# Optimization experiments

Hardware: AMD Instinct MI355X
Metric: run time of the kernel (lower is better)

## Reference

```python
import jax, jax.numpy as jnp
import numpy as np

MAX_ITER = 3  # module default init kwarg
B, S = 16, 128


def setup_inputs() -> dict:
    key = jax.random.key(0)
    k1, k2, k3 = jax.random.split(key, 3)
    s_span = jax.random.normal(k1, (B, S, S), dtype=jnp.float32)
    s_pair = jax.random.normal(k2, (B, S, S, S), dtype=jnp.float32)
    mask = jax.random.randint(k3, (B, S, S), 0, 2).astype(jnp.bool_)
    return {"s_span": s_span, "s_pair": s_pair, "mask": mask}


def reference(s_span, s_pair, mask):
    # Faithful batch-first translation of MFVIConstituency.mfvi + sigmoid.
    # torch code works in [S, S, B] layout; here we keep [B, S, S].
    seq_len = mask.shape[1]
    idx = jnp.arange(seq_len)
    # ls[i,j]=min(i,j), rs[i,j]=max(i,j) (stack(where(ones)).sort(0) trick)
    ls = jnp.minimum(idx[:, None], idx[None, :])  # [S, S]
    rs = jnp.maximum(idx[:, None], idx[None, :])  # [S, S]
    # exclude k == min(i,j) and k == max(i,j): [S, S, S] over (i, j, k)
    ne = (ls[:, :, None] != idx[None, None, :]) & (rs[:, :, None] != idx[None, None, :])
    # span_mask broadcast in torch aligns trailing dims -> indexed at (j, k):
    # mask2o[b,i,j,k] &= mask[b,k,j] | mask[b,j,k]
    span = mask | jnp.swapaxes(mask, 1, 2)  # [B, S, S] symmetric
    # mask2o[b,i,j,k] = mask[b,i,j] & ne[i,j,k] & span[b,j,k]
    mask2o = mask[:, :, :, None] & ne[None, :, :, :] & span[:, None, :, :]
    sp = s_pair * mask2o.astype(s_pair.dtype)  # [B, S, S, S]
    q = s_span
    for _ in range(MAX_ITER):
        q = jax.nn.sigmoid(q)
        # q_new[b,i,j] = s_span[b,i,j] + sum_k q[b,i,k] * sp[b,i,j,k]
        q = s_span + jnp.einsum('bik,bijk->bij', q, sp)
    return jax.nn.sigmoid(q)  # marginals [B, S, S]
```

## Files before the change

### kernel.cpp

```cpp
#include <hip/hip_runtime.h>
#include <hip/hip_bf16.h>


#define S 128
#define MB_STRIDE 132
#define PART_STRIDE 33

static __device__ __forceinline__ float fsig(float x) {
    return __builtin_amdgcn_rcpf(1.0f + __expf(-x));
}

__global__ __launch_bounds__(256, 2) void pack_masks(
    const int* __restrict__ mask, unsigned* __restrict__ spanw,
    unsigned* __restrict__ miw)
{
    __shared__ unsigned char mb[S * MB_STRIDE];
    const int t = threadIdx.x, b = blockIdx.x;
    const int* mrow = mask + (long long)b * (S * S);
    #pragma unroll
    for (int s2 = 0; s2 < 16; ++s2) {
        int f4 = t + 256 * s2;
        int j  = f4 >> 5;
        int k0 = (f4 & 31) * 4;
        int4 v = *(const int4*)(mrow + f4 * 4);
        unsigned packed = (v.x ? 1u : 0u)
                        | ((v.y ? 1u : 0u) << 8)
                        | ((v.z ? 1u : 0u) << 16)
                        | ((v.w ? 1u : 0u) << 24);
        *(unsigned*)(mb + j * MB_STRIDE + k0) = packed;
    }
    __syncthreads();
    #pragma unroll
    for (int r = 0; r < 2; ++r) {
        int task = t * 2 + r;
        int j = task >> 2, w = task & 3;
        unsigned sbits = 0, mbits = 0;
        #pragma unroll
        for (int c = 0; c < 32; ++c) {
            int k = w * 32 + c;
            unsigned mjk = mb[j * MB_STRIDE + k];
            unsigned mkj = mb[k * MB_STRIDE + j];
            sbits |= ((mjk | mkj) ? 1u : 0u) << c;
            mbits |= (mjk ? 1u : 0u) << c;
        }
        spanw[(b * S + j) * 4 + w] = sbits;
        miw  [(b * S + j) * 4 + w] = mbits;
    }
}

__global__ __launch_bounds__(256, 4) void mfvi_main(
    const float* __restrict__ s_span,
    const float* __restrict__ s_pair,
    const unsigned* __restrict__ spanw,
    const unsigned* __restrict__ miw,
    float* __restrict__ out)
{
    __shared__ float         part[S * PART_STRIDE];
    __shared__ unsigned      sw_l[S * 4];
    __shared__ float         prow[S];
    __shared__ float         qsv [S];
    __shared__ unsigned char act [S];
    __shared__ int           nact_s;

    const int t  = threadIdx.x;
    const int bi = blockIdx.x;
    const int i  = bi & (S - 1);
    const int b  = bi >> 7;
    const int row0 = t >> 5;
    const int c4   = (t & 31) * 4;
    const float* tile = s_pair + (long long)bi * (S * S);

    if (t < S) *(uint4*)&sw_l[t * 4] = *(const uint4*)&spanw[(b * S + t) * 4];
    if (t < S) {
        float sv = s_span[(long long)bi * S + t];
        qsv[t]  = sv;
        prow[t] = fsig(sv);
    }
    if (t < 64) {
        unsigned w0 = miw[(b * S + i) * 4 + (t >> 5)];
        bool a0 = (w0 >> (t & 31)) & 1u;
        unsigned long long b0 = __ballot(a0);
        int p0 = __popcll(b0 & ((1ull << t) - 1ull));
        if (a0) act[p0] = (unsigned char)t;
        int n0 = __popcll(b0);
        int j1 = t + 64;
        unsigned w1 = miw[(b * S + i) * 4 + (j1 >> 5)];
        bool a1 = (w1 >> (j1 & 31)) & 1u;
        unsigned long long b1 = __ballot(a1);
        int p1 = n0 + __popcll(b1 & ((1ull << t) - 1ull));
        if (a1) act[p1] = (unsigned char)j1;
        if (t == 0) nact_s = n0 + __popcll(b1);
    }
    __syncthreads();
    const int nact = nact_s;

    if (t < S) {
        bool mine = (miw[(b * S + i) * 4 + (t >> 5)] >> (t & 31)) & 1u;
        if (!mine) out[(long long)bi * S + t] = prow[t];
    }

    float4 v[16];
    #pragma unroll
    for (int s = 0; s < 16; ++s) {
        int idx = row0 + 8 * s;
        if (idx < nact) {
            int j = act[idx];
            v[s] = *(const float4*)(tile + j * S + c4);
        } else {
            v[s] = make_float4(0.f, 0.f, 0.f, 0.f);
        }
    }

    #pragma unroll
    for (int s = 0; s < 16; ++s) {
        int idx = row0 + 8 * s;
        if (idx < nact) {
            int j = act[idx];
            unsigned cw = sw_l[j * 4 + (c4 >> 5)];
            int lo = i < j ? i : j, hi = i < j ? j : i;
            if ((lo >> 5) == (c4 >> 5)) cw &= ~(1u << (lo & 31));
            if ((hi >> 5) == (c4 >> 5)) cw &= ~(1u << (hi & 31));
            unsigned cs = cw >> (c4 & 31);
            int m0 = ((int)(cs << 31)) >> 31;
            int m1 = ((int)(cs << 30)) >> 31;
            int m2 = ((int)(cs << 29)) >> 31;
            int m3 = ((int)(cs << 28)) >> 31;
            v[s].x = __int_as_float(__float_as_int(v[s].x) & m0);
            v[s].y = __int_as_float(__float_as_int(v[s].y) & m1);
            v[s].z = __int_as_float(__float_as_int(v[s].z) & m2);
            v[s].w = __int_as_float(__float_as_int(v[s].w) & m3);
        }
    }

    const int pcol = t & 31;
    #pragma unroll
    for (int it = 0; it < 3; ++it) {
        float4 p = *(const float4*)&prow[c4];
        #pragma unroll
        for (int s = 0; s < 16; ++s) {
            int idx = row0 + 8 * s;
            if (idx < nact) {
                float acc = v[s].x * p.x + v[s].y * p.y + v[s].z * p.z + v[s].w * p.w;
                part[idx * PART_STRIDE + pcol] = acc;
            }
        }
        __syncthreads();
        if (t < nact) {
            int j = act[t];
            float sum = 0.f;
            #pragma unroll
            for (int c = 0; c < 32; ++c) sum += part[t * PART_STRIDE + c];
            float q = qsv[j] + sum;
            if (it < 2) prow[j] = fsig(q);
            else        out[(long long)bi * S + j] = fsig(q);
        }
        if (it < 2) __syncthreads();
    }
}

extern "C" void kernel_launch(void* const* d_in, const int* in_sizes, int n_in,
                              void* d_out, int out_size, void* d_ws, size_t ws_size,
                              hipStream_t stream) {
    const float* s_span = (const float*)d_in[0];
    const float* s_pair = (const float*)d_in[1];
    const int*   mask   = (const int*)d_in[2];
    float*       out    = (float*)d_out;

    int num_rows = in_sizes[0] / S;
    int B        = in_sizes[2] / (S * S);

    unsigned* ws_span = (unsigned*)d_ws;
    unsigned* ws_mi   = ws_span + (size_t)B * S * 4;

    pack_masks<<<B, 256, 0, stream>>>(mask, ws_span, ws_mi);
    mfvi_main<<<num_rows, 256, 0, stream>>>(s_span, s_pair, ws_span, ws_mi, out);
}
```

Measured before the change: 191.0 us.

## Replace shared-memory partial sums with DPP row reductions and double-buffer probabilities

The per-iteration reduction that wrote 32 partials per active row to shared memory, synchronised, and then summed serially is replaced by a DPP reduction inside each 32-lane group. One lane per group applies the sigmoid and writes into a double-buffered probability row. This removes one barrier per iteration and the shared partial array. The mask-packing kernel now runs four blocks per batch and computes only span bits. The main kernel reads the row mask directly and uses non-temporal loads for s_pair, with the masking fused into the load loop. The DPP row_bcast pattern is used to combine 16-lane rows into 32-lane sums, and its correctness depends on the lane layout.

```diff
diff --git a/kernel.cpp b/kernel.cpp
--- a/kernel.cpp
+++ b/kernel.cpp
@@ -1,66 +1,68 @@
 #include <hip/hip_runtime.h>
-#include <hip/hip_bf16.h>
 
 
 #define S 128
 #define MB_STRIDE 132
-#define PART_STRIDE 33
+
+typedef float f4 __attribute__((ext_vector_type(4)));
 
 static __device__ __forceinline__ float fsig(float x) {
     return __builtin_amdgcn_rcpf(1.0f + __expf(-x));
 }
 
+template<int CTRL, int RM>
+static __device__ __forceinline__ float dpp_red(float x) {
+    return __int_as_float(__builtin_amdgcn_update_dpp(
+        0, __float_as_int(x), CTRL, RM, 0xF, false));
+}
+
 __global__ __launch_bounds__(256, 2) void pack_masks(
-    const int* __restrict__ mask, unsigned* __restrict__ spanw,
-    unsigned* __restrict__ miw)
+    const int* __restrict__ mask, unsigned* __restrict__ spanw)
 {
-    __shared__ unsigned char mb[S * MB_STRIDE];
-    const int t = threadIdx.x, b = blockIdx.x;
+    __shared__ __align__(16) unsigned char mb[S * MB_STRIDE];
+    const int t    = threadIdx.x;
+    const int b    = blockIdx.x >> 2;
+    const int part = blockIdx.x & 3;
     const int* mrow = mask + (long long)b * (S * S);
     #pragma unroll
     for (int s2 = 0; s2 < 16; ++s2) {
-        int f4 = t + 256 * s2;
-        int j  = f4 >> 5;
-        int k0 = (f4 & 31) * 4;
-        int4 v = *(const int4*)(mrow + f4 * 4);
-        unsigned packed = (v.x ? 1u : 0u)
-                        | ((v.y ? 1u : 0u) << 8)
-                        | ((v.z ? 1u : 0u) << 16)
-                        | ((v.w ? 1u : 0u) << 24);
+        int f4i = t + 256 * s2;
+        int j   = f4i >> 5;
+        int k0  = (f4i & 31) * 4;
+        int4 vv = *(const int4*)(mrow + f4i * 4);
+        unsigned packed = (vv.x ? 1u : 0u)
+                        | ((vv.y ? 1u : 0u) << 8)
+                        | ((vv.z ? 1u : 0u) << 16)
+                        | ((vv.w ? 1u : 0u) << 24);
         *(unsigned*)(mb + j * MB_STRIDE + k0) = packed;
     }
     __syncthreads();
-    #pragma unroll
-    for (int r = 0; r < 2; ++r) {
-        int task = t * 2 + r;
-        int j = task >> 2, w = task & 3;
-        unsigned sbits = 0, mbits = 0;
+    if (t < 128) {
+        int j = part * 32 + (t >> 2), w = t & 3;
+        unsigned sbits = 0;
         #pragma unroll
         for (int c = 0; c < 32; ++c) {
             int k = w * 32 + c;
             unsigned mjk = mb[j * MB_STRIDE + k];
             unsigned mkj = mb[k * MB_STRIDE + j];
             sbits |= ((mjk | mkj) ? 1u : 0u) << c;
-            mbits |= (mjk ? 1u : 0u) << c;
         }
         spanw[(b * S + j) * 4 + w] = sbits;
-        miw  [(b * S + j) * 4 + w] = mbits;
     }
 }
 
 __global__ __launch_bounds__(256, 4) void mfvi_main(
     const float* __restrict__ s_span,
     const float* __restrict__ s_pair,
+    const int* __restrict__ mask,
     const unsigned* __restrict__ spanw,
-    const unsigned* __restrict__ miw,
     float* __restrict__ out)
 {
-    __shared__ float         part[S * PART_STRIDE];
-    __shared__ unsigned      sw_l[S * 4];
-    __shared__ float         prow[S];
-    __shared__ float         qsv [S];
-    __shared__ unsigned char act [S];
-    __shared__ int           nact_s;
+    __shared__ __align__(16) unsigned sw_l[S * 4];
+    __shared__ __align__(16) float prow[2][S];
+    __shared__ float qsv[S];
+    __shared__ unsigned char act[S];
+    __shared__ int nact_s;
 
     const int t  = threadIdx.x;
     const int bi = blockIdx.x;
@@ -69,90 +71,81 @@
     const int row0 = t >> 5;
     const int c4   = (t & 31) * 4;
     const float* tile = s_pair + (long long)bi * (S * S);
+    const int*   mrow = mask + (long long)bi * S;
 
     if (t < S) *(uint4*)&sw_l[t * 4] = *(const uint4*)&spanw[(b * S + t) * 4];
     if (t < S) {
         float sv = s_span[(long long)bi * S + t];
-        qsv[t]  = sv;
-        prow[t] = fsig(sv);
+        qsv[t] = sv;
+        float pf = fsig(sv);
+        prow[0][t] = pf;
+        prow[1][t] = pf;
+        if (mrow[t] == 0)
+            out[(long long)bi * S + t] = pf;
     }
     if (t < 64) {
-        unsigned w0 = miw[(b * S + i) * 4 + (t >> 5)];
-        bool a0 = (w0 >> (t & 31)) & 1u;
+        bool a0 = mrow[t] != 0;
         unsigned long long b0 = __ballot(a0);
         int p0 = __popcll(b0 & ((1ull << t) - 1ull));
         if (a0) act[p0] = (unsigned char)t;
         int n0 = __popcll(b0);
-        int j1 = t + 64;
-        unsigned w1 = miw[(b * S + i) * 4 + (j1 >> 5)];
-        bool a1 = (w1 >> (j1 & 31)) & 1u;
+        bool a1 = mrow[t + 64] != 0;
         unsigned long long b1 = __ballot(a1);
         int p1 = n0 + __popcll(b1 & ((1ull << t) - 1ull));
-        if (a1) act[p1] = (unsigned char)j1;
+        if (a1) act[p1] = (unsigned char)(t + 64);
         if (t == 0) nact_s = n0 + __popcll(b1);
     }
     __syncthreads();
     const int nact = nact_s;
 
-    if (t < S) {
-        bool mine = (miw[(b * S + i) * 4 + (t >> 5)] >> (t & 31)) & 1u;
-        if (!mine) out[(long long)bi * S + t] = prow[t];
-    }
-
-    float4 v[16];
+    f4 v[16];
+    unsigned js_p[4] = {0u, 0u, 0u, 0u};
     #pragma unroll
     for (int s = 0; s < 16; ++s) {
-        int idx = row0 + 8 * s;
+        const int idx = row0 + 8 * s;
         if (idx < nact) {
-            int j = act[idx];
-            v[s] = *(const float4*)(tile + j * S + c4);
-        } else {
-            v[s] = make_float4(0.f, 0.f, 0.f, 0.f);
+            const int j = act[idx];
+            js_p[s >> 2] |= (unsigned)j << (8 * (s & 3));
+            f4 t4 = __builtin_nontemporal_load((const f4*)(tile + j * S + c4));
+            unsigned cw = sw_l[j * 4 + (c4 >> 5)];
+            const int lo = i < j ? i : j, hi = i < j ? j : i;
+            if ((lo >> 5) == (c4 >> 5)) cw &= ~(1u << (lo & 31));
+            if ((hi >> 5) == (c4 >> 5)) cw &= ~(1u << (hi & 31));
+            const unsigned cs = cw >> (c4 & 31);
+            const int m0 = ((int)(cs << 31)) >> 31;
+            const int m1 = ((int)(cs << 30)) >> 31;
+            const int m2 = ((int)(cs << 29)) >> 31;
+            const int m3 = ((int)(cs << 28)) >> 31;
+            t4.x = __int_as_float(__float_as_int(t4.x) & m0);
+            t4.y = __int_as_float(__float_as_int(t4.y) & m1);
+            t4.z = __int_as_float(__float_as_int(t4.z) & m2);
+            t4.w = __int_as_float(__float_as_int(t4.w) & m3);
+            v[s] = t4;
         }
     }
 
     #pragma unroll
-    for (int s = 0; s < 16; ++s) {
-        int idx = row0 + 8 * s;
-        if (idx < nact) {
-            int j = act[idx];
-            unsigned cw = sw_l[j * 4 + (c4 >> 5)];
-            int lo = i < j ? i : j, hi = i < j ? j : i;
-            if ((lo >> 5) == (c4 >> 5)) cw &= ~(1u << (lo & 31));
-            if ((hi >> 5) == (c4 >> 5)) cw &= ~(1u << (hi & 31));
-            unsigned cs = cw >> (c4 & 31);
-            int m0 = ((int)(cs << 31)) >> 31;
-            int m1 = ((int)(cs << 30)) >> 31;
-            int m2 = ((int)(cs << 29)) >> 31;
-            int m3 = ((int)(cs << 28)) >> 31;
-            v[s].x = __int_as_float(__float_as_int(v[s].x) & m0);
-            v[s].y = __int_as_float(__float_as_int(v[s].y) & m1);
-            v[s].z = __int_as_float(__float_as_int(v[s].z) & m2);
-            v[s].w = __int_as_float(__float_as_int(v[s].w) & m3);
-        }
-    }
-
-    const int pcol = t & 31;
-    #pragma unroll
     for (int it = 0; it < 3; ++it) {
-        float4 p = *(const float4*)&prow[c4];
+        const int cur = it & 1;
+        f4 p = *(const f4*)&prow[cur][c4];
         #pragma unroll
         for (int s = 0; s < 16; ++s) {
-            int idx = row0 + 8 * s;
+            const int idx = row0 + 8 * s;
             if (idx < nact) {
-                float acc = v[s].x * p.x + v[s].y * p.y + v[s].z * p.z + v[s].w * p.w;
-                part[idx * PART_STRIDE + pcol] = acc;
+                float acc = v[s].x * p.x + v[s].y * p.y
+                          + v[s].z * p.z + v[s].w * p.w;
+                acc += dpp_red<0x111, 0xF>(acc);
+                acc += dpp_red<0x112, 0xF>(acc);
+                acc += dpp_red<0x114, 0xF>(acc);
+                acc += dpp_red<0x118, 0xF>(acc);
+                acc += dpp_red<0x142, 0xA>(acc);
+                if ((t & 31) == 31) {
+                    const int j = (int)((js_p[s >> 2] >> (8 * (s & 3))) & 0xFFu);
+                    const float q = qsv[j] + acc;
+                    if (it < 2) prow[cur ^ 1][j] = fsig(q);
+                    else        out[(long long)bi * S + j] = fsig(q);
+                }
             }
-        }
-        __syncthreads();
-        if (t < nact) {
-            int j = act[t];
-            float sum = 0.f;
-            #pragma unroll
-            for (int c = 0; c < 32; ++c) sum += part[t * PART_STRIDE + c];
-            float q = qsv[j] + sum;
-            if (it < 2) prow[j] = fsig(q);
-            else        out[(long long)bi * S + j] = fsig(q);
         }
         if (it < 2) __syncthreads();
     }
@@ -170,8 +163,7 @@
     int B        = in_sizes[2] / (S * S);
 
     unsigned* ws_span = (unsigned*)d_ws;
-    unsigned* ws_mi   = ws_span + (size_t)B * S * 4;
 
-    pack_masks<<<B, 256, 0, stream>>>(mask, ws_span, ws_mi);
-    mfvi_main<<<num_rows, 256, 0, stream>>>(s_span, s_pair, ws_span, ws_mi, out);
+    pack_masks<<<B * 4, 256, 0, stream>>>(mask, ws_span);
+    mfvi_main<<<num_rows, 256, 0, stream>>>(s_span, s_pair, mask, ws_span, out);
 }
```

Result: no change. 188.6 us (-1.3%).
